# Performance work log

Measured on AMD Instinct MI355X. Metric: run time of the kernel, lower is better.

Reference implementation:

```python
import jax, jax.numpy as jnp
import numpy as np
from jax import lax

B, C, H, W = 16, 128, 64, 64
AUX = 2 * 128 + 20 + 1  # hybrid: edge(128)+seg(128)+pred_edge(1)+pred_seg(20)
PATCHES = [(2, 2), (4, 4)]


def conv1x1(x, w, b):
    # w: [O, I]
    return jnp.einsum('bchw,oc->bohw', x, w) + b[None, :, None, None]


def conv3x3(x, w, b, pad, dil=1):
    y = lax.conv_general_dilated(x, w, (1, 1), [(pad, pad), (pad, pad)],
                                 rhs_dilation=(dil, dil),
                                 dimension_numbers=('NCHW', 'OIHW', 'NCHW'))
    return y + b[None, :, None, None]


def layernorm_chw(x, eps=1e-5):
    # LayerNorm over [C,H,W] per sample, no affine
    mu = x.mean(axis=(1, 2, 3), keepdims=True)
    var = ((x - mu) ** 2).mean(axis=(1, 2, 3), keepdims=True)
    return (x - mu) / jnp.sqrt(var + eps)


def adn(x, aux, ew, eb, sw, sb, bw, bb):
    a = conv1x1(aux, ew, eb)
    gamma = conv1x1(a, sw, sb)
    beta = conv1x1(jnp.concatenate([x, a], axis=1), bw, bb)
    return layernorm_chw(x) * gamma + beta


def window_attn(q, k, v, ph, pw):
    b, dk, h, w = q.shape
    oh, ow = h // ph, w // pw

    def patch(t):  # [b,dk,h,w] -> [b, oh*ow, dk*ph*pw]
        t = t.reshape(b, dk, oh, ph, ow, pw)
        return t.transpose(0, 2, 4, 1, 3, 5).reshape(b, oh * ow, dk * ph * pw)

    Q, K, V = patch(q), patch(k), patch(v)
    scale = 1.0 / jnp.sqrt(jnp.asarray(Q.shape[-1], Q.dtype))
    scores = jnp.einsum('bnd,bmd->bnm', Q, K) * scale
    y = jnp.einsum('bnm,bmd->bnd', jax.nn.softmax(scores, axis=-1), V)
    y = y.reshape(b, oh, ow, dk, ph, pw).transpose(0, 3, 1, 4, 2, 5).reshape(b, dk, h, w)
    return y


def mssa_forward(p):
    (x, edge, seg, pred_edge, pred_seg,
     q_w, q_b, k_w, k_b, v_w, v_b,
     d1_embed_w, d1_embed_b, d1_scale_w, d1_scale_b, d1_bias_w, d1_bias_b,
     d2_embed_w, d2_embed_b, d2_scale_w, d2_scale_b, d2_bias_w, d2_bias_b,
     sc_w, sc_b, bi1_w, bi1_b, bi2_w, bi2_b) = p

    aux = jnp.concatenate([edge, seg, pred_edge, pred_seg], axis=1)

    q = adn(conv1x1(x, q_w, q_b), aux, d1_embed_w, d1_embed_b, d1_scale_w, d1_scale_b, d1_bias_w, d1_bias_b)
    k = adn(conv1x1(x, k_w, k_b), aux, d1_embed_w, d1_embed_b, d1_scale_w, d1_scale_b, d1_bias_w, d1_bias_b)
    v = adn(conv1x1(x, v_w, v_b), aux, d1_embed_w, d1_embed_b, d1_scale_w, d1_scale_b, d1_bias_w, d1_bias_b)

    qs = jnp.split(q, len(PATCHES), axis=1)
    ks = jnp.split(k, len(PATCHES), axis=1)
    vs = jnp.split(v, len(PATCHES), axis=1)
    outs = [window_attn(qs[i], ks[i], vs[i], PATCHES[i][1], PATCHES[i][0]) for i in range(len(PATCHES))]

    mid = x + jnp.concatenate(outs, axis=1)
    o = adn(mid, aux, d2_embed_w, d2_embed_b, d2_scale_w, d2_scale_b, d2_bias_w, d2_bias_b)
    gamma = jnp.tanh(conv3x3(o, sc_w, sc_b, pad=1))
    beta = conv3x3(jax.nn.gelu(conv3x3(o, bi1_w, bi1_b, pad=2, dil=2), approximate=False), bi2_w, bi2_b, pad=1)
    return mid * gamma + beta


def setup_inputs() -> dict:
    key = jax.random.key(0)
    ks = iter(jax.random.split(key, 40))
    nrm = lambda shape, s=1.0: jax.random.normal(next(ks), shape, jnp.float32) * s
    P = 0.02  # param init scale
    inp = {
        'x': nrm((B, C, H, W)),
        'edge': nrm((B, 128, H, W)),
        'seg': nrm((B, 128, H, W)),
        'pred_edge': jax.random.uniform(next(ks), (B, 1, H, W), jnp.float32),
        'pred_seg': jax.random.uniform(next(ks), (B, 20, H, W), jnp.float32),
        'q_w': nrm((C, C), P), 'q_b': jnp.zeros((C,), jnp.float32),
        'k_w': nrm((C, C), P), 'k_b': jnp.zeros((C,), jnp.float32),
        'v_w': nrm((C, C), P), 'v_b': jnp.zeros((C,), jnp.float32),
        'd1_embed_w': nrm((C, AUX), P), 'd1_embed_b': jnp.zeros((C,), jnp.float32),
        'd1_scale_w': nrm((C, C), P), 'd1_scale_b': jnp.ones((C,), jnp.float32),
        'd1_bias_w': nrm((C, 2 * C), P), 'd1_bias_b': jnp.zeros((C,), jnp.float32),
        'd2_embed_w': nrm((C, AUX), P), 'd2_embed_b': jnp.zeros((C,), jnp.float32),
        'd2_scale_w': nrm((C, C), P), 'd2_scale_b': jnp.ones((C,), jnp.float32),
        'd2_bias_w': nrm((C, 2 * C), P), 'd2_bias_b': jnp.zeros((C,), jnp.float32),
        'sc_w': nrm((C, C, 3, 3), P), 'sc_b': jnp.zeros((C,), jnp.float32),
        'bi1_w': nrm((C, C, 3, 3), P), 'bi1_b': jnp.zeros((C,), jnp.float32),
        'bi2_w': nrm((C, C, 3, 3), P), 'bi2_b': jnp.zeros((C,), jnp.float32),
    }
    return inp


def reference(x, edge, seg, pred_edge, pred_seg,
              q_w, q_b, k_w, k_b, v_w, v_b,
              d1_embed_w, d1_embed_b, d1_scale_w, d1_scale_b, d1_bias_w, d1_bias_b,
              d2_embed_w, d2_embed_b, d2_scale_w, d2_scale_b, d2_bias_w, d2_bias_b,
              sc_w, sc_b, bi1_w, bi1_b, bi2_w, bi2_b):
    return mssa_forward((x, edge, seg, pred_edge, pred_seg,
                         q_w, q_b, k_w, k_b, v_w, v_b,
                         d1_embed_w, d1_embed_b, d1_scale_w, d1_scale_b, d1_bias_w, d1_bias_b,
                         d2_embed_w, d2_embed_b, d2_scale_w, d2_scale_b, d2_bias_w, d2_bias_b,
                         sc_w, sc_b, bi1_w, bi1_b, bi2_w, bi2_b))
```

## Files before the change

### kernel.cpp

```cpp
#include <hip/hip_runtime.h>
#include <cstdint>

typedef unsigned short ushort_t;
typedef unsigned int uint_t;
typedef __attribute__((ext_vector_type(8))) short short8;
typedef __attribute__((ext_vector_type(4))) float f32x4;

#define MFMA16(a, b, c) __builtin_amdgcn_mfma_f32_16x16x32_bf16((a), (b), (c), 0, 0, 0)
#define SWZ(c, r) ((((c) + ((r) >> 2)) & 3))
#define INV_N 1.9073486328125e-6f

__device__ __forceinline__ ushort_t f2bf(float f) {
    uint_t u = __builtin_bit_cast(uint_t, f);
    u += 0x7FFFu + ((u >> 16) & 1u);
    return (ushort_t)(u >> 16);
}
__device__ __forceinline__ float bf2f(ushort_t h) {
    return __builtin_bit_cast(float, (uint_t)h << 16);
}

__global__ __launch_bounds__(256) void prep_w(
    ushort_t* wb, const float* qw, const float* kw, const float* vw,
    const float* ew1, const float* ew2, const float* sw1, const float* sw2,
    const float* bw1, const float* bw2,
    const float* scw, const float* b1w, const float* b2w)
{
    int idx = blockIdx.x * 256 + threadIdx.x;
    if (idx >= 663552) return;
    float v;
    if (idx < 49152) {
        int z = idx >> 14, r = idx & 16383;
        v = (z == 0 ? qw : z == 1 ? kw : vw)[r];
    } else if (idx < 122880) {
        int j = idx - 49152; int z = j / 36864; int jj = j - z * 36864;
        int o = jj / 288, k = jj - o * 288;
        v = (k < 277) ? (z ? ew2 : ew1)[o * 277 + k] : 0.f;
    } else if (idx < 155648) {
        int j = idx - 122880; int z = j >> 14;
        v = (z ? sw2 : sw1)[j & 16383];
    } else if (idx < 221184) {
        int j = idx - 155648; int z = j >> 15;
        v = (z ? bw2 : bw1)[j & 32767];
    } else {
        int j = idx - 221184;
        const float* src = j < 147456 ? scw : j < 294912 ? b1w : b2w;
        j = j % 147456;
        int tap = j >> 14, r = (j >> 7) & 127, c = j & 127;
        v = src[r * 1152 + c * 9 + tap];
    }
    wb[idx] = f2bf(v);
}

__global__ __launch_bounds__(256) void transp_x(const float* __restrict__ x, ushort_t* __restrict__ xT)
{
    __shared__ ushort_t tile[64 * 130];
    int b = blockIdx.y, p0 = blockIdx.x * 64;
    int t = threadIdx.x;
    for (int s = t; s < 8192; s += 256) {
        int c = s >> 6, p = s & 63;
        tile[p * 130 + c] = f2bf(x[((size_t)(b * 128 + c) << 12) + p0 + p]);
    }
    __syncthreads();
    for (int s = t; s < 8192; s += 256) {
        int p = s >> 7, c = s & 127;
        xT[((size_t)(b * 4096) + p0 + p) * 128 + c] = tile[p * 130 + c];
    }
}

__global__ __launch_bounds__(256) void transp_aux(const float* __restrict__ edge, const float* __restrict__ seg,
                                                  const float* __restrict__ pe, const float* __restrict__ ps,
                                                  ushort_t* __restrict__ auxT)
{
    __shared__ ushort_t tile[64 * 292];
    int b = blockIdx.y, p0 = blockIdx.x * 64;
    int t = threadIdx.x;
    for (int s = t; s < 18432; s += 256) {
        int c = s >> 6, p = s & 63;
        float v = 0.f;
        if (c < 128)       v = edge[((size_t)(b * 128 + c) << 12) + p0 + p];
        else if (c < 256)  v = seg[((size_t)(b * 128 + c - 128) << 12) + p0 + p];
        else if (c == 256) v = pe[((size_t)b << 12) + p0 + p];
        else if (c < 277)  v = ps[((size_t)(b * 20 + c - 257) << 12) + p0 + p];
        tile[p * 292 + c] = f2bf(v);
    }
    __syncthreads();
    for (int s = t; s < 18432; s += 256) {
        int p = s / 288, c = s - p * 288;
        auxT[((size_t)(b * 4096) + p0 + p) * 288 + c] = tile[p * 292 + c];
    }
}

template <int EP>
__global__ __launch_bounds__(256) void gemm_conv(
    const ushort_t* bA, int Kb1, const ushort_t* bB, size_t zBoff,
    const ushort_t* wA, int wAperZ, int NK,
    const float* b0, const float* b1, const float* b2,
    ushort_t* o0, ushort_t* o1, ushort_t* o2,
    const ushort_t* gT, float* stats, int dostats)
{
    constexpr int LDSZ = (EP == 2) ? 33792 : 16448;
    __shared__ char lds[LDSZ];
    int b = blockIdx.y, bx = blockIdx.x, z = blockIdx.z;
    int t = threadIdx.x, lane = t & 63, w = t >> 6;
    int wm = w & 1, wn = w >> 1, lo = lane & 15, quad = lane >> 4;
    int KtotA = Kb1 + (bB ? 128 : 0);
    const ushort_t* wAz = wA + (wAperZ ? (size_t)z * 128 * KtotA : 0);
    const ushort_t* bAz = bA + (size_t)z * zBoff;
    const float* bias = z == 0 ? b0 : z == 1 ? b1 : b2;
    ushort_t* outp = z == 0 ? o0 : z == 1 ? o1 : o2;

    f32x4 acc[4][4];
#pragma unroll
    for (int i = 0; i < 4; ++i)
#pragma unroll
        for (int j = 0; j < 4; ++j) acc[i][j] = (f32x4){0.f, 0.f, 0.f, 0.f};

    size_t prow = (size_t)(b * 4096 + bx * 128);
    int r0 = t >> 2, c0 = t & 3, r1 = r0 + 64;
    uint4 pfA0, pfA1, pfB0, pfB1;
    {
        pfA0 = *(const uint4*)(wAz + (size_t)r0 * KtotA + c0 * 8);
        pfA1 = *(const uint4*)(wAz + (size_t)r1 * KtotA + c0 * 8);
        int kk = c0 * 8;
        const ushort_t* s0 = (kk < Kb1) ? bAz + (prow + r0) * Kb1 + kk : bB + (prow + r0) * 128 + (kk - Kb1);
        const ushort_t* s1 = (kk < Kb1) ? bAz + (prow + r1) * Kb1 + kk : bB + (prow + r1) * 128 + (kk - Kb1);
        pfB0 = *(const uint4*)s0;
        pfB1 = *(const uint4*)s1;
    }
    for (int ck = 0; ck < NK; ++ck) {
        __syncthreads();
        *(uint4*)(lds + r0 * 64 + SWZ(c0, r0) * 16) = pfA0;
        *(uint4*)(lds + r1 * 64 + SWZ(c0, r1) * 16) = pfA1;
        *(uint4*)(lds + 8192 + r0 * 64 + SWZ(c0, r0) * 16) = pfB0;
        *(uint4*)(lds + 8192 + r1 * 64 + SWZ(c0, r1) * 16) = pfB1;
        __syncthreads();
        if (ck + 1 < NK) {
            int k0 = (ck + 1) * 32;
            pfA0 = *(const uint4*)(wAz + (size_t)r0 * KtotA + k0 + c0 * 8);
            pfA1 = *(const uint4*)(wAz + (size_t)r1 * KtotA + k0 + c0 * 8);
            int kk = k0 + c0 * 8;
            const ushort_t* s0 = (kk < Kb1) ? bAz + (prow + r0) * Kb1 + kk : bB + (prow + r0) * 128 + (kk - Kb1);
            const ushort_t* s1 = (kk < Kb1) ? bAz + (prow + r1) * Kb1 + kk : bB + (prow + r1) * 128 + (kk - Kb1);
            pfB0 = *(const uint4*)s0;
            pfB1 = *(const uint4*)s1;
        }
        short8 af[4];
#pragma unroll
        for (int mt = 0; mt < 4; ++mt) {
            int row = wm * 64 + mt * 16 + lo;
            af[mt] = *(const short8*)(lds + row * 64 + SWZ(quad, row) * 16);
        }
#pragma unroll
        for (int nt = 0; nt < 4; ++nt) {
            int n = wn * 64 + nt * 16 + lo;
            short8 bf = *(const short8*)(lds + 8192 + n * 64 + SWZ(quad, n) * 16);
#pragma unroll
            for (int mt = 0; mt < 4; ++mt) acc[mt][nt] = MFMA16(af[mt], bf, acc[mt][nt]);
        }
    }

    float mean = 0.f, rstd = 0.f;
    if (EP >= 2) {
        int slot = (EP == 3) ? 3 : z;
        float s0 = stats[(slot * 16 + b) * 2], s1 = stats[(slot * 16 + b) * 2 + 1];
        mean = s0 * INV_N;
        rstd = rsqrtf(fmaxf(s1 * INV_N - mean * mean, 0.f) + 1e-5f);
    }
    float lsum = 0.f, lss = 0.f;
    if (EP == 2) {
        __syncthreads();
        ushort_t* Cs = (ushort_t*)lds;
#pragma unroll
        for (int mt = 0; mt < 4; ++mt)
#pragma unroll
            for (int nt = 0; nt < 4; ++nt) {
                int oo0 = wm * 64 + mt * 16 + quad * 4;
                int pp = wn * 64 + nt * 16 + lo;
                size_t tbase = (prow + pp) * 128 + oo0;
                ushort4 tv = *(const ushort4*)(bAz + tbase);
                ushort4 gv = *(const ushort4*)(gT + tbase);
#pragma unroll
                for (int r = 0; r < 4; ++r) {
                    float v = acc[mt][nt][r] + bias[oo0 + r]
                            + (bf2f((&tv.x)[r]) - mean) * rstd * bf2f((&gv.x)[r]);
                    Cs[(oo0 + r) * 132 + pp] = f2bf(v);
                }
            }
        __syncthreads();
        int y0 = bx * 2;
        if (z < 2) {
            for (int s = t; s < 1024; s += 256) {
                int n_l = s >> 5, fq = s & 31;
                ushort_t tmp[8];
#pragma unroll
                for (int e = 0; e < 8; ++e) {
                    int f = fq * 8 + e;
                    tmp[e] = Cs[(f >> 2) * 132 + ((f >> 1) & 1) * 64 + n_l * 2 + (f & 1)];
                }
                uint4 ov;
                ov.x = (uint_t)tmp[0] | ((uint_t)tmp[1] << 16);
                ov.y = (uint_t)tmp[2] | ((uint_t)tmp[3] << 16);
                ov.z = (uint_t)tmp[4] | ((uint_t)tmp[5] << 16);
                ov.w = (uint_t)tmp[6] | ((uint_t)tmp[7] << 16);
                *(uint4*)(outp + ((size_t)(b * 1024 + (y0 >> 1) * 32 + n_l) << 8) + fq * 8) = ov;
            }
            int n0 = (y0 >> 2) << 4, py0 = y0 & 3;
            for (int s = t; s < 2048; s += 256) {
                int n_l = s & 15, c = (s >> 4) & 63, py = s >> 10;
                ushort_t tmp[4];
#pragma unroll
                for (int px = 0; px < 4; ++px)
                    tmp[px] = Cs[(64 + c) * 132 + py * 64 + n_l * 4 + px];
                uint2 ov;
                ov.x = (uint_t)tmp[0] | ((uint_t)tmp[1] << 16);
                ov.y = (uint_t)tmp[2] | ((uint_t)tmp[3] << 16);
                *(uint2*)(outp + 4194304u + ((size_t)(b * 256 + n0 + n_l) << 10) + c * 16 + (py0 + py) * 4) = ov;
            }
        } else {
            int n0h0 = (y0 >> 1) * 32;
            for (int s = t; s < 2048; s += 256) {
                int f = s >> 3, j = s & 7;
                int oo = f >> 2, py = (f >> 1) & 1, px = f & 1;
                ushort_t tmp[4];
#pragma unroll
                for (int i2 = 0; i2 < 4; ++i2)
                    tmp[i2] = Cs[oo * 132 + py * 64 + (j * 4 + i2) * 2 + px];
                uint2 ov;
                ov.x = (uint_t)tmp[0] | ((uint_t)tmp[1] << 16);
                ov.y = (uint_t)tmp[2] | ((uint_t)tmp[3] << 16);
                *(uint2*)(outp + ((size_t)(b * 256 + f) << 10) + n0h0 + j * 4) = ov;
            }
            int n0 = (y0 >> 2) << 4, py0 = y0 & 3;
            for (int s = t; s < 2048; s += 256) {
                int fi = s >> 2, j = s & 3;
                int c = fi >> 3, py = (fi >> 2) & 1, px = fi & 3;
                int f = c * 16 + (py0 + py) * 4 + px;
                ushort_t tmp[4];
#pragma unroll
                for (int i2 = 0; i2 < 4; ++i2)
                    tmp[i2] = Cs[(64 + c) * 132 + py * 64 + (j * 4 + i2) * 4 + px];
                uint2 ov;
                ov.x = (uint_t)tmp[0] | ((uint_t)tmp[1] << 16);
                ov.y = (uint_t)tmp[2] | ((uint_t)tmp[3] << 16);
                *(uint2*)(outp + 4194304u + ((size_t)(b * 1024 + f) << 8) + n0 + j * 4) = ov;
            }
        }
    } else {
#pragma unroll
        for (int mt = 0; mt < 4; ++mt)
#pragma unroll
            for (int nt = 0; nt < 4; ++nt) {
                int oo0 = wm * 64 + mt * 16 + quad * 4;
                int pp = wn * 64 + nt * 16 + lo;
                size_t tbase = (prow + pp) * 128 + oo0;
                float vv[4];
#pragma unroll
                for (int r = 0; r < 4; ++r) vv[r] = acc[mt][nt][r] + bias[oo0 + r];
                if (EP == 3) {
                    ushort4 tv = *(const ushort4*)(bAz + tbase);
                    ushort4 gv = *(const ushort4*)(gT + tbase);
#pragma unroll
                    for (int r = 0; r < 4; ++r)
                        vv[r] += (bf2f((&tv.x)[r]) - mean) * rstd * bf2f((&gv.x)[r]);
                }
                ushort4 st = {f2bf(vv[0]), f2bf(vv[1]), f2bf(vv[2]), f2bf(vv[3])};
                *(ushort4*)(outp + tbase) = st;
                if (EP == 0 && dostats) {
#pragma unroll
                    for (int r = 0; r < 4; ++r) { lsum += vv[r]; lss += vv[r] * vv[r]; }
                }
            }
    }
    if (EP == 0 && dostats) {
#pragma unroll
        for (int o2 = 32; o2 >= 1; o2 >>= 1) { lsum += __shfl_xor(lsum, o2); lss += __shfl_xor(lss, o2); }
        __syncthreads();
        float* red = (float*)lds;
        if (lane == 0) { red[w * 2] = lsum; red[w * 2 + 1] = lss; }
        __syncthreads();
        if (t == 0) {
            atomicAdd(&stats[(z * 16 + b) * 2], red[0] + red[2] + red[4] + red[6]);
            atomicAdd(&stats[(z * 16 + b) * 2 + 1], red[1] + red[3] + red[5] + red[7]);
        }
    }
}

template <int EP>
__global__ __launch_bounds__(256) void gemm_attn(
    const ushort_t* A, size_t aBS, const ushort_t* Bm, size_t bBS,
    int Ka, int NK, float scale,
    ushort_t* sout, size_t soBS, int soNb,
    const ushort_t* xT, ushort_t* midT, float* stats)
{
    constexpr int LDSZ = (EP >= 1) ? 33792 : 16448;
    __shared__ char lds[LDSZ];
    int b = blockIdx.z, my = blockIdx.y, nx = blockIdx.x;
    int t = threadIdx.x, lane = t & 63, w = t >> 6;
    int wm = w & 1, wn = w >> 1, lo = lane & 15, quad = lane >> 4;

    f32x4 acc[4][4];
#pragma unroll
    for (int i = 0; i < 4; ++i)
#pragma unroll
// ... 97 lines not shown
#pragma unroll
    for (int o2 = 32; o2 >= 1; o2 >>= 1) { lsum += __shfl_xor(lsum, o2); lss += __shfl_xor(lss, o2); }
    __syncthreads();
    float* red = (float*)lds;
    if (lane == 0) { red[w * 2] = lsum; red[w * 2 + 1] = lss; }
    __syncthreads();
    if (t == 0) {
        atomicAdd(&stats[(3 * 16 + b) * 2], red[0] + red[2] + red[4] + red[6]);
        atomicAdd(&stats[(3 * 16 + b) * 2 + 1], red[1] + red[3] + red[5] + red[7]);
    }
}

__global__ __launch_bounds__(256) void softmax_k(ushort_t* SP)
{
    int wid = blockIdx.x * 4 + (threadIdx.x >> 6);
    int lane = threadIdx.x & 63;
    ushort_t* row;
    int PL;
    if (wid < 16384) { row = SP + ((size_t)wid << 10); PL = 16; }
    else { int r2 = wid - 16384; row = SP + 16777216u + ((size_t)r2 << 8); PL = 4; }
    float v[16];
    float mx = -1e30f;
    for (int i = 0; i < PL; ++i) { v[i] = bf2f(row[lane + (i << 6)]); mx = fmaxf(mx, v[i]); }
#pragma unroll
    for (int o = 32; o >= 1; o >>= 1) mx = fmaxf(mx, __shfl_xor(mx, o));
    float sum = 0.f;
    for (int i = 0; i < PL; ++i) { v[i] = __expf(v[i] - mx); sum += v[i]; }
#pragma unroll
    for (int o = 32; o >= 1; o >>= 1) sum += __shfl_xor(sum, o);
    float inv = 1.f / sum;
    for (int i = 0; i < PL; ++i) row[lane + (i << 6)] = f2bf(v[i] * inv);
}

template <int DIL, int EP>
__global__ __launch_bounds__(256) void conv3x3_mfma(
    const ushort_t* __restrict__ inT, const ushort_t* __restrict__ wt, const float* __restrict__ bias,
    void* __restrict__ out, const ushort_t* __restrict__ midT, const ushort_t* __restrict__ g3T)
{
    constexpr int NR = 2 + 2 * DIL;
    __shared__ char lds[24576 + NR * 68 * 64];
    char* Braw = lds + 24576;
    int b = blockIdx.y;
    int y0 = blockIdx.x * 2;
    int t = threadIdx.x, lane = t & 63, w = t >> 6;
    int wm = w & 1, wn = w >> 1, lo = lane & 15, quad = lane >> 4;

    f32x4 acc[4][4];
#pragma unroll
    for (int i = 0; i < 4; ++i)
#pragma unroll
        for (int j = 0; j < 4; ++j) acc[i][j] = (f32x4){0.f, 0.f, 0.f, 0.f};

    for (int cc = 0; cc < 4; ++cc) {
        __syncthreads();
        constexpr int NSLOT = NR * 68 * 4;
        for (int s = t; s < NSLOT; s += 256) {
            int c4 = s & 3;
            int pr = s >> 2;
            int xx = pr % 68, rr = pr / 68;
            int ys = y0 - DIL + rr;
            int ix = xx - DIL;
            uint4 v = {0u, 0u, 0u, 0u};
            if (ys >= 0 && ys < 64 && (unsigned)ix < 64u)
                v = *(const uint4*)(inT + (size_t)(b * 4096 + ys * 64 + ix) * 128 + cc * 32 + c4 * 8);
            *(uint4*)(Braw + pr * 64 + SWZ(c4, pr) * 16) = v;
        }
        for (int ky = 0; ky < 3; ++ky) {
            __syncthreads();
            for (int s = t; s < 1536; s += 256) {
                int kx = s >> 9, r = (s >> 2) & 127, c = s & 3;
                uint4 v = *(const uint4*)(wt + ((size_t)((ky * 3 + kx) * 128 + r) << 7) + cc * 32 + c * 8);
                *(uint4*)(lds + kx * 8192 + r * 64 + SWZ(c, r) * 16) = v;
            }
            __syncthreads();
#pragma unroll
            for (int kx = 0; kx < 3; ++kx) {
                short8 af[4];
#pragma unroll
                for (int mt = 0; mt < 4; ++mt) {
                    int row = wm * 64 + mt * 16 + lo;
                    af[mt] = *(const short8*)(lds + kx * 8192 + row * 64 + SWZ(quad, row) * 16);
                }
#pragma unroll
                for (int nt = 0; nt < 4; ++nt) {
                    int n = wn * 64 + nt * 16 + lo;
                    int pr = ((n >> 6) + ky * DIL) * 68 + (n & 63) + kx * DIL;
                    short8 bf = *(const short8*)(Braw + pr * 64 + SWZ(quad, pr) * 16);
#pragma unroll
                    for (int mt = 0; mt < 4; ++mt) acc[mt][nt] = MFMA16(af[mt], bf, acc[mt][nt]);
                }
            }
        }
    }
#pragma unroll
    for (int mt = 0; mt < 4; ++mt)
#pragma unroll
        for (int nt = 0; nt < 4; ++nt) {
            int oo0 = wm * 64 + mt * 16 + quad * 4;
            int pp = wn * 64 + nt * 16 + lo;
            int sp = (y0 + (pp >> 6)) * 64 + (pp & 63);
            size_t tbase = ((size_t)(b * 4096) + sp) * 128 + oo0;
            if (EP == 0) {
                ushort4 st;
#pragma unroll
                for (int r = 0; r < 4; ++r)
                    (&st.x)[r] = f2bf(tanhf(acc[mt][nt][r] + bias[oo0 + r]));
                *(ushort4*)((ushort_t*)out + tbase) = st;
            } else if (EP == 1) {
                ushort4 st;
#pragma unroll
                for (int r = 0; r < 4; ++r) {
                    float v = acc[mt][nt][r] + bias[oo0 + r];
                    (&st.x)[r] = f2bf(0.5f * v * (1.f + erff(v * 0.70710678118654752f)));
                }
                *(ushort4*)((ushort_t*)out + tbase) = st;
            } else {
                ushort4 mv = *(const ushort4*)(midT + tbase);
                ushort4 gv = *(const ushort4*)(g3T + tbase);
#pragma unroll
                for (int r = 0; r < 4; ++r) {
                    int oo = oo0 + r;
                    size_t off = ((size_t)(b * 128 + oo) << 12) + sp;
                    ((float*)out)[off] = bf2f((&mv.x)[r]) * bf2f((&gv.x)[r]) + acc[mt][nt][r] + bias[oo];
                }
            }
        }
}

extern "C" void kernel_launch(void* const* d_in, const int* in_sizes, int n_in,
                              void* d_out, int out_size, void* d_ws, size_t ws_size,
                              hipStream_t stream)
{
    const float* x    = (const float*)d_in[0];
    const float* edge = (const float*)d_in[1];
    const float* seg  = (const float*)d_in[2];
    const float* pe   = (const float*)d_in[3];
    const float* ps   = (const float*)d_in[4];
    const float* q_w  = (const float*)d_in[5];  const float* q_b  = (const float*)d_in[6];
    const float* k_w  = (const float*)d_in[7];  const float* k_b  = (const float*)d_in[8];
    const float* v_w  = (const float*)d_in[9];  const float* v_b  = (const float*)d_in[10];
    const float* d1_ew = (const float*)d_in[11]; const float* d1_eb = (const float*)d_in[12];
    const float* d1_sw = (const float*)d_in[13]; const float* d1_sb = (const float*)d_in[14];
    const float* d1_bw = (const float*)d_in[15]; const float* d1_bb = (const float*)d_in[16];
    const float* d2_ew = (const float*)d_in[17]; const float* d2_eb = (const float*)d_in[18];
    const float* d2_sw = (const float*)d_in[19]; const float* d2_sb = (const float*)d_in[20];
    const float* d2_bw = (const float*)d_in[21]; const float* d2_bb = (const float*)d_in[22];
    const float* sc_w  = (const float*)d_in[23]; const float* sc_b  = (const float*)d_in[24];
    const float* bi1_w = (const float*)d_in[25]; const float* bi1_b = (const float*)d_in[26];
    const float* bi2_w = (const float*)d_in[27]; const float* bi2_b = (const float*)d_in[28];

    char* ws = (char*)d_ws;
    ushort_t* wb = (ushort_t*)ws;
    float* stats = (float*)(ws + 1327360);
    char* RA = ws + 1327872;
    char* RB = RA + 37748736;
    char* RC = RB + 16777216;
    char* RD = RC + 50331648;
    char* RE = RD + 33554432;
    char* RF = RE + 33554432;
    char* RG = RF + 33554432;

    ushort_t* auxT = (ushort_t*)RA;
    ushort_t* SP0  = (ushort_t*)RA;
    ushort_t* xT   = (ushort_t*)RB;
    ushort_t* q0T  = (ushort_t*)RC;
    ushort_t* midT = (ushort_t*)RC;
    ushort_t* oT   = (ushort_t*)(RC + 16777216);
    ushort_t* a1T  = (ushort_t*)RD;
    ushort_t* g1   = (ushort_t*)RE;
    ushort_t* g2   = g1 + 8388608;
    ushort_t* Qp   = (ushort_t*)RF;
    ushort_t* Kp   = Qp + 8388608;
    ushort_t* g3   = (ushort_t*)RF;
    ushort_t* VT   = (ushort_t*)RG;
    ushort_t* tT   = (ushort_t*)RG;
    const size_t ZB = 8388608;

    dim3 blk(256);

    hipMemsetAsync(stats, 0, 512, stream);
    prep_w<<<2592, blk, 0, stream>>>(wb, q_w, k_w, v_w, d1_ew, d2_ew, d1_sw, d2_sw, d1_bw, d2_bw, sc_w, bi1_w, bi2_w);
    transp_x<<<dim3(64, 16), blk, 0, stream>>>(x, xT);
    transp_aux<<<dim3(64, 16), blk, 0, stream>>>(edge, seg, pe, ps, auxT);

    gemm_conv<0><<<dim3(32, 16, 2), blk, 0, stream>>>(auxT, 288, nullptr, 0, wb + 49152, 1, 9,
        d1_eb, d2_eb, nullptr, a1T, a1T + ZB, nullptr, nullptr, stats, 0);
    gemm_conv<0><<<dim3(32, 16, 2), blk, 0, stream>>>(a1T, 128, nullptr, ZB, wb + 122880, 1, 4,
        d1_sb, d2_sb, nullptr, g1, g2, nullptr, nullptr, stats, 0);
    gemm_conv<0><<<dim3(32, 16, 3), blk, 0, stream>>>(xT, 128, nullptr, 0, wb, 1, 4,
        q_b, k_b, v_b, q0T, q0T + ZB, q0T + 2 * ZB, nullptr, stats, 1);
    gemm_conv<2><<<dim3(32, 16, 3), blk, 0, stream>>>(q0T, 128, a1T, ZB, wb + 155648, 0, 8,
        d1_bb, d1_bb, d1_bb, Qp, Kp, VT, g1, stats, 0);

    gemm_attn<0><<<dim3(8, 8, 16), blk, 0, stream>>>(Qp, 262144, Kp, 262144, 256, 8, 0.0625f,
        SP0, 1048576, 1024, nullptr, nullptr, stats);
    gemm_attn<0><<<dim3(2, 2, 16), blk, 0, stream>>>(Qp + 4194304, 262144, Kp + 4194304, 262144, 1024, 32, 0.03125f,
        SP0 + 16777216, 65536, 256, nullptr, nullptr, stats);
    softmax_k<<<5120, blk, 0, stream>>>(SP0);
    gemm_attn<1><<<dim3(2, 8, 16), blk, 0, stream>>>(SP0, 1048576, VT, 262144, 1024, 32, 1.f,
        nullptr, 0, 0, xT, midT, stats);
    gemm_attn<2><<<dim3(8, 2, 16), blk, 0, stream>>>(SP0 + 16777216, 65536, VT + 4194304, 262144, 256, 8, 1.f,
        nullptr, 0, 0, xT, midT, stats);

    gemm_conv<3><<<dim3(32, 16, 1), blk, 0, stream>>>(midT, 128, a1T + ZB, 0, wb + 155648 + 32768, 0, 8,
        d2_bb, nullptr, nullptr, oT, nullptr, nullptr, g2, stats, 0);

    conv3x3_mfma<1, 0><<<dim3(32, 16), blk, 0, stream>>>(oT, wb + 221184, sc_b, g3, nullptr, nullptr);
    conv3x3_mfma<2, 1><<<dim3(32, 16), blk, 0, stream>>>(oT, wb + 368640, bi1_b, tT, nullptr, nullptr);
    conv3x3_mfma<1, 2><<<dim3(32, 16), blk, 0, stream>>>(tT, wb + 516096, bi2_b, d_out, midT, g3);
}
```

Measured before the change: 710.3 us.

## Fold embed conv into scale/bias weights, vectorize transposes, merge 3x3 convs

Precomputes combined weights (scale_w·embed_w and bias_w[:,C:]·embed_w) and biases so gamma and the aux half of beta come straight from the aux input in one 4-way GEMM. This removes the intermediate a1 activation and halves the K of the beta GEMMs. Transpose kernels now use float4 loads and 128-bit stores. The EP2 epilogue switches to 2D spatial tiles with vectorized window writes, and the two convs sharing the oT input run in one launch. The trade-off is extra weight-prep kernels and a larger K=288 GEMM per output, and folding the weights in bf16 changes rounding.

```diff
diff --git a/kernel.cpp b/kernel.cpp
--- a/kernel.cpp
+++ b/kernel.cpp
@@ -9,6 +9,9 @@
 #define MFMA16(a, b, c) __builtin_amdgcn_mfma_f32_16x16x32_bf16((a), (b), (c), 0, 0, 0)
 #define SWZ(c, r) ((((c) + ((r) >> 2)) & 3))
 #define INV_N 1.9073486328125e-6f
+
+struct P4 { ushort_t* p[4]; };
+struct B4 { const float* b[4]; };
 
 __device__ __forceinline__ ushort_t f2bf(float f) {
     uint_t u = __builtin_bit_cast(uint_t, f);
@@ -51,19 +54,86 @@
     wb[idx] = f2bf(v);
 }
 
+__global__ __launch_bounds__(256) void combine_w(ushort_t* wc, const ushort_t* wb)
+{
+    __shared__ float ews[128 * 33];
+    __shared__ ushort_t Ws[128 * 130];
+    int z = blockIdx.y, nt = blockIdx.x, n0 = nt * 32;
+    int t = threadIdx.x;
+    const ushort_t* wew = wb + 49152;
+    const ushort_t* wsw = wb + 122880;
+    const ushort_t* wbw = wb + 155648;
+    const ushort_t* W; int wstr, wof;
+    if (z == 0)      { W = wsw;         wstr = 128; wof = 0; }
+    else if (z == 1) { W = wbw;         wstr = 256; wof = 128; }
+    else if (z == 2) { W = wsw + 16384; wstr = 128; wof = 0; }
+    else             { W = wbw + 32768; wstr = 256; wof = 128; }
+    const ushort_t* E = wew + (z >= 2 ? 36864 : 0);
+    for (int s = t; s < 16384; s += 256) {
+        int c = s & 127, o = s >> 7;
+        Ws[c * 130 + o] = W[o * wstr + wof + c];
+    }
+    for (int s = t; s < 4096; s += 256) {
+        int c = s >> 5, n = s & 31;
+        ews[c * 33 + n] = bf2f(E[c * 288 + n0 + n]);
+    }
+    __syncthreads();
+    int o = t & 127, nh = t >> 7;
+    float acc[16];
+#pragma unroll
+    for (int i = 0; i < 16; ++i) acc[i] = 0.f;
+    for (int c = 0; c < 128; ++c) {
+        float wv = bf2f(Ws[c * 130 + o]);
+#pragma unroll
+        for (int i = 0; i < 16; ++i) acc[i] += wv * ews[c * 33 + nh * 16 + i];
+    }
+#pragma unroll
+    for (int i = 0; i < 16; ++i)
+        wc[(size_t)(z * 128 + o) * 288 + n0 + nh * 16 + i] = f2bf(acc[i]);
+}
+
+__global__ __launch_bounds__(512) void combine_bias(
+    float* bc, const float* sw1, const float* bw1, const float* sw2, const float* bw2,
+    const float* eb1, const float* eb2, const float* sb1, const float* bb1,
+    const float* sb2, const float* bb2)
+{
+    int t = threadIdx.x; int z = t >> 7, o = t & 127;
+    const float* W; int wstr, wof; const float* eb; float add;
+    if (z == 0)      { W = sw1; wstr = 128; wof = 0;   eb = eb1; add = sb1[o]; }
+    else if (z == 1) { W = bw1; wstr = 256; wof = 128; eb = eb1; add = bb1[o]; }
+    else if (z == 2) { W = sw2; wstr = 128; wof = 0;   eb = eb2; add = sb2[o]; }
+    else             { W = bw2; wstr = 256; wof = 128; eb = eb2; add = bb2[o]; }
+    float s = add;
+    for (int c = 0; c < 128; ++c) s += W[o * wstr + wof + c] * eb[c];
+    bc[t] = s;
+}
+
 __global__ __launch_bounds__(256) void transp_x(const float* __restrict__ x, ushort_t* __restrict__ xT)
 {
     __shared__ ushort_t tile[64 * 130];
     int b = blockIdx.y, p0 = blockIdx.x * 64;
     int t = threadIdx.x;
-    for (int s = t; s < 8192; s += 256) {
-        int c = s >> 6, p = s & 63;
-        tile[p * 130 + c] = f2bf(x[((size_t)(b * 128 + c) << 12) + p0 + p]);
+#pragma unroll
+    for (int i = 0; i < 8; ++i) {
+        int s = t + i * 256;
+        int c = s >> 4, p4 = (s & 15) * 4;
+        float4 f = *(const float4*)(x + ((size_t)(b * 128 + c) << 12) + p0 + p4);
+        tile[(p4 + 0) * 130 + c] = f2bf(f.x);
+        tile[(p4 + 1) * 130 + c] = f2bf(f.y);
+        tile[(p4 + 2) * 130 + c] = f2bf(f.z);
+        tile[(p4 + 3) * 130 + c] = f2bf(f.w);
     }
     __syncthreads();
-    for (int s = t; s < 8192; s += 256) {
-        int p = s >> 7, c = s & 127;
-        xT[((size_t)(b * 4096) + p0 + p) * 128 + c] = tile[p * 130 + c];
+#pragma unroll
+    for (int i = 0; i < 4; ++i) {
+        int s = t + i * 256;
+        int p = s >> 4, c8 = (s & 15) * 8;
+        ushort_t v[8];
+#pragma unroll
+        for (int e = 0; e < 8; ++e) v[e] = tile[p * 130 + c8 + e];
+        uint4 ov = {(uint_t)v[0] | ((uint_t)v[1] << 16), (uint_t)v[2] | ((uint_t)v[3] << 16),
+                    (uint_t)v[4] | ((uint_t)v[5] << 16), (uint_t)v[6] | ((uint_t)v[7] << 16)};
+        *(uint4*)(xT + ((size_t)(b * 4096) + p0 + p) * 128 + c8) = ov;
     }
 }
 
@@ -74,40 +144,52 @@
     __shared__ ushort_t tile[64 * 292];
     int b = blockIdx.y, p0 = blockIdx.x * 64;
     int t = threadIdx.x;
-    for (int s = t; s < 18432; s += 256) {
-        int c = s >> 6, p = s & 63;
-        float v = 0.f;
-        if (c < 128)       v = edge[((size_t)(b * 128 + c) << 12) + p0 + p];
-        else if (c < 256)  v = seg[((size_t)(b * 128 + c - 128) << 12) + p0 + p];
-        else if (c == 256) v = pe[((size_t)b << 12) + p0 + p];
-        else if (c < 277)  v = ps[((size_t)(b * 20 + c - 257) << 12) + p0 + p];
-        tile[p * 292 + c] = f2bf(v);
+#pragma unroll
+    for (int i = 0; i < 18; ++i) {
+        int s = t + i * 256;
+        int c = s >> 4, p4 = (s & 15) * 4;
+        float4 f = {0.f, 0.f, 0.f, 0.f};
+        if (c < 128)       f = *(const float4*)(edge + ((size_t)(b * 128 + c) << 12) + p0 + p4);
+        else if (c < 256)  f = *(const float4*)(seg + ((size_t)(b * 128 + c - 128) << 12) + p0 + p4);
+        else if (c == 256) f = *(const float4*)(pe + ((size_t)b << 12) + p0 + p4);
+        else if (c < 277)  f = *(const float4*)(ps + ((size_t)(b * 20 + c - 257) << 12) + p0 + p4);
+        tile[(p4 + 0) * 292 + c] = f2bf(f.x);
+        tile[(p4 + 1) * 292 + c] = f2bf(f.y);
+        tile[(p4 + 2) * 292 + c] = f2bf(f.z);
+        tile[(p4 + 3) * 292 + c] = f2bf(f.w);
     }
     __syncthreads();
-    for (int s = t; s < 18432; s += 256) {
-        int p = s / 288, c = s - p * 288;
-        auxT[((size_t)(b * 4096) + p0 + p) * 288 + c] = tile[p * 292 + c];
+#pragma unroll
+    for (int i = 0; i < 9; ++i) {
+        int s = t + i * 256;
+        int p = s / 36, c8 = (s % 36) * 8;
+        ushort_t v[8];
+#pragma unroll
+        for (int e = 0; e < 8; ++e) v[e] = tile[p * 292 + c8 + e];
+        uint4 ov = {(uint_t)v[0] | ((uint_t)v[1] << 16), (uint_t)v[2] | ((uint_t)v[3] << 16),
+                    (uint_t)v[4] | ((uint_t)v[5] << 16), (uint_t)v[6] | ((uint_t)v[7] << 16)};
+        *(uint4*)(auxT + ((size_t)(b * 4096) + p0 + p) * 288 + c8) = ov;
     }
 }
 
 template <int EP>
 __global__ __launch_bounds__(256) void gemm_conv(
-    const ushort_t* bA, int Kb1, const ushort_t* bB, size_t zBoff,
-    const ushort_t* wA, int wAperZ, int NK,
-    const float* b0, const float* b1, const float* b2,
-    ushort_t* o0, ushort_t* o1, ushort_t* o2,
-    const ushort_t* gT, float* stats, int dostats)
+    const ushort_t* bA, int Kb1, size_t zBoff,
+    const ushort_t* wA, int wstride, int wAperZ, int NK,
+    B4 bias4, P4 out4, const ushort_t* gT, const ushort_t* betT,
+    float* stats, int dostats)
 {
     constexpr int LDSZ = (EP == 2) ? 33792 : 16448;
     __shared__ char lds[LDSZ];
     int b = blockIdx.y, bx = blockIdx.x, z = blockIdx.z;
     int t = threadIdx.x, lane = t & 63, w = t >> 6;
     int wm = w & 1, wn = w >> 1, lo = lane & 15, quad = lane >> 4;
-    int KtotA = Kb1 + (bB ? 128 : 0);
-    const ushort_t* wAz = wA + (wAperZ ? (size_t)z * 128 * KtotA : 0);
+    const ushort_t* wAz = wA + (wAperZ ? (size_t)z * 128 * wstride : 0);
     const ushort_t* bAz = bA + (size_t)z * zBoff;
-    const float* bias = z == 0 ? b0 : z == 1 ? b1 : b2;
-    ushort_t* outp = z == 0 ? o0 : z == 1 ? o1 : o2;
+    ushort_t* outp = out4.p[z];
+    size_t bbase = (size_t)b * 4096;
+    int y0 = 0, x0 = 0;
+    if (EP == 2) { y0 = (bx >> 1) * 4; x0 = (bx & 1) * 32; }
 
     f32x4 acc[4][4];
 #pragma unroll
@@ -115,18 +197,21 @@
 #pragma unroll
         for (int j = 0; j < 4; ++j) acc[i][j] = (f32x4){0.f, 0.f, 0.f, 0.f};
 
-    size_t prow = (size_t)(b * 4096 + bx * 128);
     int r0 = t >> 2, c0 = t & 3, r1 = r0 + 64;
-    uint4 pfA0, pfA1, pfB0, pfB1;
-    {
-        pfA0 = *(const uint4*)(wAz + (size_t)r0 * KtotA + c0 * 8);
-        pfA1 = *(const uint4*)(wAz + (size_t)r1 * KtotA + c0 * 8);
-        int kk = c0 * 8;
-        const ushort_t* s0 = (kk < Kb1) ? bAz + (prow + r0) * Kb1 + kk : bB + (prow + r0) * 128 + (kk - Kb1);
-        const ushort_t* s1 = (kk < Kb1) ? bAz + (prow + r1) * Kb1 + kk : bB + (prow + r1) * 128 + (kk - Kb1);
-        pfB0 = *(const uint4*)s0;
-        pfB1 = *(const uint4*)s1;
-    }
+    int gp0, gp1;
+    if (EP == 2) {
+        gp0 = (y0 + (r0 >> 5)) * 64 + x0 + (r0 & 31);
+        gp1 = (y0 + (r1 >> 5)) * 64 + x0 + (r1 & 31);
+    } else {
+        gp0 = bx * 128 + r0;
+        gp1 = bx * 128 + r1;
+    }
+    const ushort_t* bRow0 = bAz + (bbase + gp0) * Kb1;
+    const ushort_t* bRow1 = bAz + (bbase + gp1) * Kb1;
+    uint4 pfA0 = *(const uint4*)(wAz + (size_t)r0 * wstride + c0 * 8);
+    uint4 pfA1 = *(const uint4*)(wAz + (size_t)r1 * wstride + c0 * 8);
+    uint4 pfB0 = *(const uint4*)(bRow0 + c0 * 8);
+    uint4 pfB1 = *(const uint4*)(bRow1 + c0 * 8);
     for (int ck = 0; ck < NK; ++ck) {
         __syncthreads();
         *(uint4*)(lds + r0 * 64 + SWZ(c0, r0) * 16) = pfA0;
@@ -136,13 +221,10 @@
         __syncthreads();
         if (ck + 1 < NK) {
             int k0 = (ck + 1) * 32;
-            pfA0 = *(const uint4*)(wAz + (size_t)r0 * KtotA + k0 + c0 * 8);
-            pfA1 = *(const uint4*)(wAz + (size_t)r1 * KtotA + k0 + c0 * 8);
-            int kk = k0 + c0 * 8;
-            const ushort_t* s0 = (kk < Kb1) ? bAz + (prow + r0) * Kb1 + kk : bB + (prow + r0) * 128 + (kk - Kb1);
-            const ushort_t* s1 = (kk < Kb1) ? bAz + (prow + r1) * Kb1 + kk : bB + (prow + r1) * 128 + (kk - Kb1);
-            pfB0 = *(const uint4*)s0;
-            pfB1 = *(const uint4*)s1;
+            pfA0 = *(const uint4*)(wAz + (size_t)r0 * wstride + k0 + c0 * 8);
+            pfA1 = *(const uint4*)(wAz + (size_t)r1 * wstride + k0 + c0 * 8);
+            pfB0 = *(const uint4*)(bRow0 + k0 + c0 * 8);
+            pfB1 = *(const uint4*)(bRow1 + k0 + c0 * 8);
         }
         short8 af[4];
 #pragma unroll
@@ -176,73 +258,72 @@
             for (int nt = 0; nt < 4; ++nt) {
                 int oo0 = wm * 64 + mt * 16 + quad * 4;
                 int pp = wn * 64 + nt * 16 + lo;
-                size_t tbase = (prow + pp) * 128 + oo0;
+                int gp = (y0 + (pp >> 5)) * 64 + x0 + (pp & 31);
+                size_t tbase = (bbase + gp) * 128 + oo0;
                 ushort4 tv = *(const ushort4*)(bAz + tbase);
                 ushort4 gv = *(const ushort4*)(gT + tbase);
+                ushort4 bv = *(const ushort4*)(betT + tbase);
 #pragma unroll
                 for (int r = 0; r < 4; ++r) {
-                    float v = acc[mt][nt][r] + bias[oo0 + r]
+                    float v = acc[mt][nt][r] + bf2f((&bv.x)[r])
                             + (bf2f((&tv.x)[r]) - mean) * rstd * bf2f((&gv.x)[r]);
                     Cs[(oo0 + r) * 132 + pp] = f2bf(v);
                 }
             }
         __syncthreads();
-        int y0 = bx * 2;
         if (z < 2) {
             for (int s = t; s < 1024; s += 256) {
                 int n_l = s >> 5, fq = s & 31;
+                int ypair = n_l >> 4, xp = n_l & 15;
                 ushort_t tmp[8];
 #pragma unroll
                 for (int e = 0; e < 8; ++e) {
                     int f = fq * 8 + e;
-                    tmp[e] = Cs[(f >> 2) * 132 + ((f >> 1) & 1) * 64 + n_l * 2 + (f & 1)];
-                }
-                uint4 ov;
-                ov.x = (uint_t)tmp[0] | ((uint_t)tmp[1] << 16);
-                ov.y = (uint_t)tmp[2] | ((uint_t)tmp[3] << 16);
-                ov.z = (uint_t)tmp[4] | ((uint_t)tmp[5] << 16);
-                ov.w = (uint_t)tmp[6] | ((uint_t)tmp[7] << 16);
-                *(uint4*)(outp + ((size_t)(b * 1024 + (y0 >> 1) * 32 + n_l) << 8) + fq * 8) = ov;
-            }
-            int n0 = (y0 >> 2) << 4, py0 = y0 & 3;
-            for (int s = t; s < 2048; s += 256) {
-                int n_l = s & 15, c = (s >> 4) & 63, py = s >> 10;
-                ushort_t tmp[4];
-#pragma unroll
-                for (int px = 0; px < 4; ++px)
-                    tmp[px] = Cs[(64 + c) * 132 + py * 64 + n_l * 4 + px];
-                uint2 ov;
-                ov.x = (uint_t)tmp[0] | ((uint_t)tmp[1] << 16);
-                ov.y = (uint_t)tmp[2] | ((uint_t)tmp[3] << 16);
-                *(uint2*)(outp + 4194304u + ((size_t)(b * 256 + n0 + n_l) << 10) + c * 16 + (py0 + py) * 4) = ov;
+                    int c = f >> 2, py = (f >> 1) & 1, px = f & 1;
+                    tmp[e] = Cs[c * 132 + (ypair * 2 + py) * 32 + xp * 2 + px];
+                }
+                int n = ((y0 >> 1) + ypair) * 32 + (x0 >> 1) + xp;
+                uint4 ov = {(uint_t)tmp[0] | ((uint_t)tmp[1] << 16), (uint_t)tmp[2] | ((uint_t)tmp[3] << 16),
+                            (uint_t)tmp[4] | ((uint_t)tmp[5] << 16), (uint_t)tmp[6] | ((uint_t)tmp[7] << 16)};
+                *(uint4*)(outp + ((size_t)(b * 1024 + n) << 8) + fq * 8) = ov;
+            }
+            for (int s = t; s < 1024; s += 256) {
+                int n_l = s >> 7, fq = s & 127;
+                ushort_t tmp[8];
+#pragma unroll
+                for (int e = 0; e < 8; ++e) {
+                    int f = fq * 8 + e;
+                    int c = f >> 4, py = (f >> 2) & 3, px = f & 3;
+                    tmp[e] = Cs[(64 + c) * 132 + py * 32 + n_l * 4 + px];
+                }
+                int n = (y0 >> 2) * 16 + (x0 >> 2) + n_l;
+                uint4 ov = {(uint_t)tmp[0] | ((uint_t)tmp[1] << 16), (uint_t)tmp[2] | ((uint_t)tmp[3] << 16),
+                            (uint_t)tmp[4] | ((uint_t)tmp[5] << 16), (uint_t)tmp[6] | ((uint_t)tmp[7] << 16)};
+                *(uint4*)(outp + 4194304u + ((size_t)(b * 256 + n) << 10) + fq * 8) = ov;
             }
         } else {
-            int n0h0 = (y0 >> 1) * 32;
             for (int s = t; s < 2048; s += 256) {
                 int f = s >> 3, j = s & 7;
-                int oo = f >> 2, py = (f >> 1) & 1, px = f & 1;
+                int ypair = j >> 2, xq = j & 3;
+                int c = f >> 2, py = (f >> 1) & 1, px = f & 1;
                 ushort_t tmp[4];
 #pragma unroll
                 for (int i2 = 0; i2 < 4; ++i2)
-                    tmp[i2] = Cs[oo * 132 + py * 64 + (j * 4 + i2) * 2 + px];
-                uint2 ov;
-                ov.x = (uint_t)tmp[0] | ((uint_t)tmp[1] << 16);
-                ov.y = (uint_t)tmp[2] | ((uint_t)tmp[3] << 16);
-                *(uint2*)(outp + ((size_t)(b * 256 + f) << 10) + n0h0 + j * 4) = ov;
-            }
-            int n0 = (y0 >> 2) << 4, py0 = y0 & 3;
+                    tmp[i2] = Cs[c * 132 + (ypair * 2 + py) * 32 + (xq * 4 + i2) * 2 + px];
+                int m0 = ((y0 >> 1) + ypair) * 32 + (x0 >> 1) + xq * 4;
+                uint2 ov = {(uint_t)tmp[0] | ((uint_t)tmp[1] << 16), (uint_t)tmp[2] | ((uint_t)tmp[3] << 16)};
+                *(uint2*)(outp + ((size_t)(b * 256 + f) << 10) + m0) = ov;
+            }
             for (int s = t; s < 2048; s += 256) {
-                int fi = s >> 2, j = s & 3;
-                int c = fi >> 3, py = (fi >> 2) & 1, px = fi & 3;
-                int f = c * 16 + (py0 + py) * 4 + px;
+                int f = s >> 1, j = s & 1;
+                int c = f >> 4, py = (f >> 2) & 3, px = f & 3;
                 ushort_t tmp[4];
 #pragma unroll
                 for (int i2 = 0; i2 < 4; ++i2)
-                    tmp[i2] = Cs[(64 + c) * 132 + py * 64 + (j * 4 + i2) * 4 + px];
-                uint2 ov;
-                ov.x = (uint_t)tmp[0] | ((uint_t)tmp[1] << 16);
-                ov.y = (uint_t)tmp[2] | ((uint_t)tmp[3] << 16);
-                *(uint2*)(outp + 4194304u + ((size_t)(b * 1024 + f) << 8) + n0 + j * 4) = ov;
+                    tmp[i2] = Cs[(64 + c) * 132 + py * 32 + (j * 4 + i2) * 4 + px];
+                int m0 = (y0 >> 2) * 16 + (x0 >> 2) + j * 4;
+                uint2 ov = {(uint_t)tmp[0] | ((uint_t)tmp[1] << 16), (uint_t)tmp[2] | ((uint_t)tmp[3] << 16)};
+                *(uint2*)(outp + 4194304u + ((size_t)(b * 1024 + f) << 8) + m0) = ov;
             }
         }
     } else {
@@ -252,23 +333,26 @@
             for (int nt = 0; nt < 4; ++nt) {
                 int oo0 = wm * 64 + mt * 16 + quad * 4;
                 int pp = wn * 64 + nt * 16 + lo;
-                size_t tbase = (prow + pp) * 128 + oo0;
+                size_t tbase = (bbase + bx * 128 + pp) * 128 + oo0;
                 float vv[4];
-#pragma unroll
-                for (int r = 0; r < 4; ++r) vv[r] = acc[mt][nt][r] + bias[oo0 + r];
-                if (EP == 3) {
+                if (EP == 0) {
+#pragma unroll
+                    for (int r = 0; r < 4; ++r) vv[r] = acc[mt][nt][r] + bias4.b[z][oo0 + r];
+                    if (dostats) {
+#pragma unroll
+                        for (int r = 0; r < 4; ++r) { lsum += vv[r]; lss += vv[r] * vv[r]; }
+                    }
+                } else {
                     ushort4 tv = *(const ushort4*)(bAz + tbase);
                     ushort4 gv = *(const ushort4*)(gT + tbase);
+                    ushort4 bv = *(const ushort4*)(betT + tbase);
 #pragma unroll
                     for (int r = 0; r < 4; ++r)
-                        vv[r] += (bf2f((&tv.x)[r]) - mean) * rstd * bf2f((&gv.x)[r]);
+                        vv[r] = acc[mt][nt][r] + bf2f((&bv.x)[r])
+                              + (bf2f((&tv.x)[r]) - mean) * rstd * bf2f((&gv.x)[r]);
                 }
                 ushort4 st = {f2bf(vv[0]), f2bf(vv[1]), f2bf(vv[2]), f2bf(vv[3])};
                 *(ushort4*)(outp + tbase) = st;
-                if (EP == 0 && dostats) {
-#pragma unroll
-                    for (int r = 0; r < 4; ++r) { lsum += vv[r]; lss += vv[r] * vv[r]; }
-                }
             }
     }
     if (EP == 0 && dostats) {
@@ -432,15 +516,19 @@
     for (int i = 0; i < PL; ++i) row[lane + (i << 6)] = f2bf(v[i] * inv);
 }
 
-template <int DIL, int EP>
-__global__ __launch_bounds__(256) void conv3x3_mfma(
-    const ushort_t* __restrict__ inT, const ushort_t* __restrict__ wt, const float* __restrict__ bias,
-    void* __restrict__ out, const ushort_t* __restrict__ midT, const ushort_t* __restrict__ g3T)
-{
-    constexpr int NR = 2 + 2 * DIL;
-    __shared__ char lds[24576 + NR * 68 * 64];
+__global__ __launch_bounds__(256) void conv3x3_dual(
+    const ushort_t* __restrict__ inT, const ushort_t* __restrict__ wtA, const ushort_t* __restrict__ wtB,
+    const float* __restrict__ biasA, const float* __restrict__ biasB,
+    ushort_t* __restrict__ outA, ushort_t* __restrict__ outB)
+{
+    __shared__ char lds[24576 + 8 * 68 * 64];
     char* Braw = lds + 24576;
-    int b = blockIdx.y;
+    int b = blockIdx.y, z = blockIdx.z;
+    int dil = 1 + z;
+    int NRr = 2 + 2 * dil;
+    const ushort_t* wt = z ? wtB : wtA;
+    const float* bias = z ? biasB : biasA;
+    ushort_t* out = z ? outB : outA;
     int y0 = blockIdx.x * 2;
     int t = threadIdx.x, lane = t & 63, w = t >> 6;
     int wm = w & 1, wn = w >> 1, lo = lane & 15, quad = lane >> 4;
@@ -453,13 +541,13 @@
 
     for (int cc = 0; cc < 4; ++cc) {
         __syncthreads();
-        constexpr int NSLOT = NR * 68 * 4;
+        int NSLOT = NRr * 68 * 4;
         for (int s = t; s < NSLOT; s += 256) {
             int c4 = s & 3;
             int pr = s >> 2;
             int xx = pr % 68, rr = pr / 68;
-            int ys = y0 - DIL + rr;
-            int ix = xx - DIL;
+            int ys = y0 - dil + rr;
+            int ix = xx - dil;
             uint4 v = {0u, 0u, 0u, 0u};
             if (ys >= 0 && ys < 64 && (unsigned)ix < 64u)
                 v = *(const uint4*)(inT + (size_t)(b * 4096 + ys * 64 + ix) * 128 + cc * 32 + c4 * 8);
@@ -484,7 +572,7 @@
 #pragma unroll
                 for (int nt = 0; nt < 4; ++nt) {
                     int n = wn * 64 + nt * 16 + lo;
-                    int pr = ((n >> 6) + ky * DIL) * 68 + (n & 63) + kx * DIL;
+                    int pr = ((n >> 6) + ky * dil) * 68 + (n & 63) + kx * dil;
                     short8 bf = *(const short8*)(Braw + pr * 64 + SWZ(quad, pr) * 16);
 #pragma unroll
                     for (int mt = 0; mt < 4; ++mt) acc[mt][nt] = MFMA16(af[mt], bf, acc[mt][nt]);
@@ -500,29 +588,90 @@
             int pp = wn * 64 + nt * 16 + lo;
             int sp = (y0 + (pp >> 6)) * 64 + (pp & 63);
             size_t tbase = ((size_t)(b * 4096) + sp) * 128 + oo0;
-            if (EP == 0) {
-                ushort4 st;
-#pragma unroll
-                for (int r = 0; r < 4; ++r)
-                    (&st.x)[r] = f2bf(tanhf(acc[mt][nt][r] + bias[oo0 + r]));
-                *(ushort4*)((ushort_t*)out + tbase) = st;
-            } else if (EP == 1) {
-                ushort4 st;
-#pragma unroll
-                for (int r = 0; r < 4; ++r) {
-                    float v = acc[mt][nt][r] + bias[oo0 + r];
-                    (&st.x)[r] = f2bf(0.5f * v * (1.f + erff(v * 0.70710678118654752f)));
-                }
-                *(ushort4*)((ushort_t*)out + tbase) = st;
-            } else {
-                ushort4 mv = *(const ushort4*)(midT + tbase);
-                ushort4 gv = *(const ushort4*)(g3T + tbase);
-#pragma unroll
-                for (int r = 0; r < 4; ++r) {
-                    int oo = oo0 + r;
-                    size_t off = ((size_t)(b * 128 + oo) << 12) + sp;
-                    ((float*)out)[off] = bf2f((&mv.x)[r]) * bf2f((&gv.x)[r]) + acc[mt][nt][r] + bias[oo];
-                }
+            ushort4 st;
+#pragma unroll
+            for (int r = 0; r < 4; ++r) {
+                float v = acc[mt][nt][r] + bias[oo0 + r];
+                if (z == 0) v = tanhf(v);
+                else        v = 0.5f * v * (1.f + erff(v * 0.70710678118654752f));
+                (&st.x)[r] = f2bf(v);
+            }
+            *(ushort4*)(out + tbase) = st;
+        }
+}
+
+__global__ __launch_bounds__(256) void conv3x3_final(
+    const ushort_t* __restrict__ inT, const ushort_t* __restrict__ wt, const float* __restrict__ bias,
+    float* __restrict__ out, const ushort_t* __restrict__ midT, const ushort_t* __restrict__ g3T)
+{
+    __shared__ char lds[24576 + 4 * 68 * 64];
+    char* Braw = lds + 24576;
+    int b = blockIdx.y;
+    int y0 = blockIdx.x * 2;
+    int t = threadIdx.x, lane = t & 63, w = t >> 6;
+    int wm = w & 1, wn = w >> 1, lo = lane & 15, quad = lane >> 4;
+
+    f32x4 acc[4][4];
+#pragma unroll
+    for (int i = 0; i < 4; ++i)
+#pragma unroll
+        for (int j = 0; j < 4; ++j) acc[i][j] = (f32x4){0.f, 0.f, 0.f, 0.f};
+
+    for (int cc = 0; cc < 4; ++cc) {
+        __syncthreads();
+        for (int s = t; s < 1088; s += 256) {
+            int c4 = s & 3;
+            int pr = s >> 2;
+            int xx = pr % 68, rr = pr / 68;
+            int ys = y0 - 1 + rr;
+            int ix = xx - 1;
+            uint4 v = {0u, 0u, 0u, 0u};
+            if (ys >= 0 && ys < 64 && (unsigned)ix < 64u)
+                v = *(const uint4*)(inT + (size_t)(b * 4096 + ys * 64 + ix) * 128 + cc * 32 + c4 * 8);
+            *(uint4*)(Braw + pr * 64 + SWZ(c4, pr) * 16) = v;
+        }
+        for (int ky = 0; ky < 3; ++ky) {
+            __syncthreads();
+            for (int s = t; s < 1536; s += 256) {
+                int kx = s >> 9, r = (s >> 2) & 127, c = s & 3;
+                uint4 v = *(const uint4*)(wt + ((size_t)((ky * 3 + kx) * 128 + r) << 7) + cc * 32 + c * 8);
+                *(uint4*)(lds + kx * 8192 + r * 64 + SWZ(c, r) * 16) = v;
+            }
+            __syncthreads();
+#pragma unroll
+            for (int kx = 0; kx < 3; ++kx) {
+                short8 af[4];
+#pragma unroll
+                for (int mt = 0; mt < 4; ++mt) {
+                    int row = wm * 64 + mt * 16 + lo;
+                    af[mt] = *(const short8*)(lds + kx * 8192 + row * 64 + SWZ(quad, row) * 16);
+                }
+#pragma unroll
+                for (int nt = 0; nt < 4; ++nt) {
+                    int n = wn * 64 + nt * 16 + lo;
+                    int pr = ((n >> 6) + ky) * 68 + (n & 63) + kx;
+                    short8 bf = *(const short8*)(Braw + pr * 64 + SWZ(quad, pr) * 16);
+#pragma unroll
+                    for (int mt = 0; mt < 4; ++mt) acc[mt][nt] = MFMA16(af[mt], bf, acc[mt][nt]);
+                }
+            }
+        }
+    }
+#pragma unroll
+    for (int mt = 0; mt < 4; ++mt)
+#pragma unroll
+        for (int nt = 0; nt < 4; ++nt) {
+            int oo0 = wm * 64 + mt * 16 + quad * 4;
+            int pp = wn * 64 + nt * 16 + lo;
+            int sp = (y0 + (pp >> 6)) * 64 + (pp & 63);
+            size_t tbase = ((size_t)(b * 4096) + sp) * 128 + oo0;
+            ushort4 mv = *(const ushort4*)(midT + tbase);
+            ushort4 gv = *(const ushort4*)(g3T + tbase);
+#pragma unroll
+            for (int r = 0; r < 4; ++r) {
+                int oo = oo0 + r;
+                size_t off = ((size_t)(b * 128 + oo) << 12) + sp;
+                out[off] = bf2f((&mv.x)[r]) * bf2f((&gv.x)[r]) + acc[mt][nt][r] + bias[oo];
             }
         }
 }
@@ -551,14 +700,18 @@
 
     char* ws = (char*)d_ws;
     ushort_t* wb = (ushort_t*)ws;
-    float* stats = (float*)(ws + 1327360);
-    char* RA = ws + 1327872;
+    ushort_t* wc = (ushort_t*)(ws + 1327360);
+    float* bc    = (float*)(ws + 1622272);
+    float* stats = (float*)(ws + 1624320);
+    char* RA = ws + 1703936;
     char* RB = RA + 37748736;
     char* RC = RB + 16777216;
     char* RD = RC + 50331648;
-    char* RE = RD + 33554432;
-    char* RF = RE + 33554432;
-    char* RG = RF + 33554432;
+    char* RE = RD + 16777216;
+    char* RF = RE + 16777216;
+    char* RG = RF + 16777216;
+    char* RH = RG + 16777216;
+    char* RI = RH + 33554432;
 
     ushort_t* auxT = (ushort_t*)RA;
     ushort_t* SP0  = (ushort_t*)RA;
@@ -566,31 +719,32 @@
     ushort_t* q0T  = (ushort_t*)RC;
     ushort_t* midT = (ushort_t*)RC;
     ushort_t* oT   = (ushort_t*)(RC + 16777216);
-    ushort_t* a1T  = (ushort_t*)RD;
-    ushort_t* g1   = (ushort_t*)RE;
-    ushort_t* g2   = g1 + 8388608;
-    ushort_t* Qp   = (ushort_t*)RF;
+    ushort_t* g1   = (ushort_t*)RD;
+    ushort_t* g3   = (ushort_t*)RD;
+    ushort_t* betA1= (ushort_t*)RE;
+    ushort_t* g2   = (ushort_t*)RF;
+    ushort_t* betA2= (ushort_t*)RG;
+    ushort_t* Qp   = (ushort_t*)RH;
     ushort_t* Kp   = Qp + 8388608;
-    ushort_t* g3   = (ushort_t*)RF;
-    ushort_t* VT   = (ushort_t*)RG;
-    ushort_t* tT   = (ushort_t*)RG;
+    ushort_t* VT   = (ushort_t*)RI;
+    ushort_t* tT   = (ushort_t*)RI;
     const size_t ZB = 8388608;
 
     dim3 blk(256);
 
     hipMemsetAsync(stats, 0, 512, stream);
     prep_w<<<2592, blk, 0, stream>>>(wb, q_w, k_w, v_w, d1_ew, d2_ew, d1_sw, d2_sw, d1_bw, d2_bw, sc_w, bi1_w, bi2_w);
+    combine_bias<<<1, 512, 0, stream>>>(bc, d1_sw, d1_bw, d2_sw, d2_bw, d1_eb, d2_eb, d1_sb, d1_bb, d2_sb, d2_bb);
+    combine_w<<<dim3(9, 4), blk, 0, stream>>>(wc, wb);
     transp_x<<<dim3(64, 16), blk, 0, stream>>>(x, xT);
     transp_aux<<<dim3(64, 16), blk, 0, stream>>>(edge, seg, pe, ps, auxT);
 
-    gemm_conv<0><<<dim3(32, 16, 2), blk, 0, stream>>>(auxT, 288, nullptr, 0, wb + 49152, 1, 9,
-        d1_eb, d2_eb, nullptr, a1T, a1T + ZB, nullptr, nullptr, stats, 0);
-    gemm_conv<0><<<dim3(32, 16, 2), blk, 0, stream>>>(a1T, 128, nullptr, ZB, wb + 122880, 1, 4,
-        d1_sb, d2_sb, nullptr, g1, g2, nullptr, nullptr, stats, 0);
-    gemm_conv<0><<<dim3(32, 16, 3), blk, 0, stream>>>(xT, 128, nullptr, 0, wb, 1, 4,
-        q_b, k_b, v_b, q0T, q0T + ZB, q0T + 2 * ZB, nullptr, stats, 1);
-    gemm_conv<2><<<dim3(32, 16, 3), blk, 0, stream>>>(q0T, 128, a1T, ZB, wb + 155648, 0, 8,
-        d1_bb, d1_bb, d1_bb, Qp, Kp, VT, g1, stats, 0);
+    gemm_conv<0><<<dim3(32, 16, 4), blk, 0, stream>>>(auxT, 288, 0, wc, 288, 1, 9,
+        B4{{bc, bc + 128, bc + 256, bc + 384}}, P4{{g1, betA1, g2, betA2}}, nullptr, nullptr, stats, 0);
+    gemm_conv<0><<<dim3(32, 16, 3), blk, 0, stream>>>(xT, 128, 0, wb, 128, 1, 4,
+        B4{{q_b, k_b, v_b, nullptr}}, P4{{q0T, q0T + ZB, q0T + 2 * ZB, nullptr}}, nullptr, nullptr, stats, 1);
+    gemm_conv<2><<<dim3(32, 16, 3), blk, 0, stream>>>(q0T, 128, ZB, wb + 155648, 256, 0, 4,
+        B4{{nullptr, nullptr, nullptr, nullptr}}, P4{{Qp, Kp, VT, nullptr}}, g1, betA1, stats, 0);
 
     gemm_attn<0><<<dim3(8, 8, 16), blk, 0, stream>>>(Qp, 262144, Kp, 262144, 256, 8, 0.0625f,
         SP0, 1048576, 1024, nullptr, nullptr, stats);
@@ -602,10 +756,9 @@
     gemm_attn<2><<<dim3(8, 2, 16), blk, 0, stream>>>(SP0 + 16777216, 65536, VT + 4194304, 262144, 256, 8, 1.f,
         nullptr, 0, 0, xT, midT, stats);
 
-    gemm_conv<3><<<dim3(32, 16, 1), blk, 0, stream>>>(midT, 128, a1T + ZB, 0, wb + 155648 + 32768, 0, 8,
-        d2_bb, nullptr, nullptr, oT, nullptr, nullptr, g2, stats, 0);
-
-    conv3x3_mfma<1, 0><<<dim3(32, 16), blk, 0, stream>>>(oT, wb + 221184, sc_b, g3, nullptr, nullptr);
-    conv3x3_mfma<2, 1><<<dim3(32, 16), blk, 0, stream>>>(oT, wb + 368640, bi1_b, tT, nullptr, nullptr);
-    conv3x3_mfma<1, 2><<<dim3(32, 16), blk, 0, stream>>>(tT, wb + 516096, bi2_b, d_out, midT, g3);
-}
+    gemm_conv<3><<<dim3(32, 16, 1), blk, 0, stream>>>(midT, 128, 0, wb + 155648 + 32768, 256, 0, 4,
+        B4{{nullptr, nullptr, nullptr, nullptr}}, P4{{oT, nullptr, nullptr, nullptr}}, g2, betA2, stats, 0);
+
+    conv3x3_dual<<<dim3(32, 16, 2), blk, 0, stream>>>(oT, wb + 221184, wb + 368640, sc_b, bi1_b, g3, tT);
+    conv3x3_final<<<dim3(32, 16), blk, 0, stream>>>(tT, wb + 516096, bi2_b, (float*)d_out, midT, g3);
+}
```

Result: no change. 702.1 us (-1.1%).
